# Kernel tuning notes

Hardware: AMD Instinct MI355X
Metric: run time of the kernel (lower is better)

## Reference

```python
import jax, jax.numpy as jnp
import numpy as np

M = 8      # num_modules
H = 128    # hidden_size per module
IN = 512   # input_size
MH = M * H

def _block_mask():
    # mask[mi*H:(mi+1)*H, mi*H:] = 1 (module mi reads modules >= mi)
    m = np.zeros((MH, MH), dtype=np.float32)
    for mi in range(M):
        m[mi*H:(mi+1)*H, mi*H:] = 1.0
    return jnp.asarray(m)

def _active_sizes(T):
    # number of active modules at step t: t=0 -> M, else min(M, trailing_zeros(t)+1)
    sizes = []
    for t in range(T):
        ma = 0
        while t % (2 ** ma) == 0 and ma < M:
            ma += 1
        sizes.append(ma * H)
    return jnp.asarray(np.array(sizes, dtype=np.int32))

def setup_inputs() -> dict:
    key = jax.random.key(0)
    k1, k2, k3, k4 = jax.random.split(key, 4)
    T, B = 256, 128
    scale = 1.0 / np.sqrt(MH)
    x = jax.random.normal(k1, (T, B, IN), dtype=jnp.float32)
    h_prev = jnp.zeros((B, MH), dtype=jnp.float32)
    Wxh = jax.random.normal(k2, (MH, IN), dtype=jnp.float32) * scale
    Whh = jax.random.normal(k3, (MH, MH), dtype=jnp.float32) * scale
    bh = jax.random.normal(k4, (MH,), dtype=jnp.float32) * scale
    return {"x": x, "h_prev": h_prev, "Wxh": Wxh, "Whh": Whh, "bh": bh}

def reference(x, h_prev, Wxh, Whh, bh):
    T = x.shape[0]
    mask = _block_mask()
    Whh_m = Whh * mask  # clockwork block-triangular mask, reapplied as in torch
    thresholds = _active_sizes(T)          # [T] active hidden width per step
    idx = jnp.arange(MH)

    # Precompute input projections for all timesteps: [T, B, MH]
    xW = jnp.einsum('tbi,hi->tbh', x, Wxh)

    def step(h, inp):
        xw_t, thr = inp
        # full-width update; rows < thr equal the torch sliced-matmul result
        h_full = h @ Whh_m.T + xw_t + bh
        h_new = jnp.where(idx < thr, h_full, h)
        return h_new, h_new

    h_last, out = jax.lax.scan(step, h_prev, (xW, thresholds))
    return (out, h_last)
```

## Files before the change

kernel.cpp:

```cpp
#include <hip/hip_runtime.h>
#include <hip/hip_bf16.h>


#define TT 256
#define BB 128
#define INW 512
#define HH 128
#define MHW 1024

typedef __bf16 bf16x8 __attribute__((ext_vector_type(8)));
typedef __bf16 bf16x4 __attribute__((ext_vector_type(4)));
typedef float f32x4 __attribute__((ext_vector_type(4)));

__constant__ unsigned int c_hmod_off[8] = {
    0u, 4194304u, 6291456u, 7340032u, 7864320u, 8126464u, 8257536u, 8323072u};

__device__ __forceinline__ int active_thr(int t) {
    int ma = (t == 0) ? 8 : min(__ffs(t), 8);
    return ma * HH;
}

__device__ __forceinline__ unsigned short f2bf(float f) {
    union { float f; unsigned int u; } v{f};
    unsigned int r = v.u + 0x7FFFu + ((v.u >> 16) & 1u);
    return (unsigned short)(r >> 16);
}
__device__ __forceinline__ unsigned int pack2(float lo, float hi) {
    return (unsigned int)f2bf(lo) | ((unsigned int)f2bf(hi) << 16);
}
__device__ __forceinline__ float bf2f(unsigned short u) {
    union { unsigned int i; float f; } v;
    v.i = ((unsigned int)u) << 16;
    return v.f;
}

__device__ __forceinline__ void gld_lds16(const void* g, char* l) {
    __builtin_amdgcn_global_load_lds(
        (const __attribute__((address_space(1))) void*)g,
        (__attribute__((address_space(3))) void*)l, 16, 0, 0);
}

__device__ __forceinline__ bf16x8 frag_ld(const char* tile, int row, int ks, int lane) {
    int off = (row * 128 + ks * 64 + (lane >> 4) * 16) ^ ((row & 7) << 4);
    return *reinterpret_cast<const bf16x8*>(tile + off);
}

__device__ __forceinline__ bf16x8 frag_ld_f32(const char* tile, int row, int ks, int g) {
    int off = ((row << 8) + ks * 128 + g * 32) ^ ((row & 7) << 4);
    f32x4 a = *reinterpret_cast<const f32x4*>(tile + off);
    f32x4 b = *reinterpret_cast<const f32x4*>(tile + (off ^ 16));
    bf16x8 u;
    u[0] = (__bf16)a[0]; u[1] = (__bf16)a[1]; u[2] = (__bf16)a[2]; u[3] = (__bf16)a[3];
    u[4] = (__bf16)b[0]; u[5] = (__bf16)b[1]; u[6] = (__bf16)b[2]; u[7] = (__bf16)b[3];
    return u;
}

__global__ __launch_bounds__(256) void k_xw(const float* __restrict__ x,
                                            const float* __restrict__ Wxh,
                                            const float* __restrict__ bh,
                                            float* __restrict__ xwb) {
    __shared__ char ldsW[2][32768];
    __shared__ char ldsX[2][16384];
    int id = blockIdx.x >> 1, half = blockIdx.x & 1;
    int rt = 0, rem = id;
    while (rem >= (256 >> rt)) { rem -= 256 >> rt; ++rt; }
    int t = rem << rt;

    int tid = threadIdx.x, lane = tid & 63, wid = tid >> 6;
    int l15 = lane & 15, g = lane >> 4;
    int wr = (wid >> 1) * 64, wc = (wid & 1) * 32;

    const float* gW[8];
    const float* gX[4];
    {
        int kb = (lane & 15) * 16;
#pragma unroll
        for (int i = 0; i < 8; ++i) {
            int row = i * 16 + wid * 4 + (lane >> 4);
            int kf = (kb ^ ((row & 7) << 4)) >> 2;
            gW[i] = Wxh + (size_t)(rt * 128 + row) * INW + kf;
        }
#pragma unroll
        for (int i = 0; i < 4; ++i) {
            int row = i * 16 + wid * 4 + (lane >> 4);
            int kf = (kb ^ ((row & 7) << 4)) >> 2;
            gX[i] = x + ((size_t)t * BB + half * 64 + row) * INW + kf;
        }
    }
#pragma unroll
    for (int i = 0; i < 8; ++i)
        gld_lds16(gW[i], &ldsW[0][0] + i * 4096 + wid * 1024);
#pragma unroll
    for (int i = 0; i < 4; ++i)
        gld_lds16(gX[i], &ldsX[0][0] + i * 4096 + wid * 1024);

    f32x4 acc[4][2] = {};
    for (int c = 0; c < 8; ++c) {
        int cur = c & 1;
        __syncthreads();
        if (c < 7) {
#pragma unroll
            for (int i = 0; i < 8; ++i)
                gld_lds16(gW[i] + (c + 1) * 64,
                          &ldsW[cur ^ 1][0] + i * 4096 + wid * 1024);
#pragma unroll
            for (int i = 0; i < 4; ++i)
                gld_lds16(gX[i] + (c + 1) * 64,
                          &ldsX[cur ^ 1][0] + i * 4096 + wid * 1024);
        }
#pragma unroll
        for (int ks = 0; ks < 2; ++ks) {
            bf16x8 fa[4], fb[2];
#pragma unroll
            for (int i = 0; i < 4; ++i)
                fa[i] = frag_ld_f32(&ldsW[cur][0], wr + i * 16 + l15, ks, g);
#pragma unroll
            for (int j = 0; j < 2; ++j)
                fb[j] = frag_ld_f32(&ldsX[cur][0], wc + j * 16 + l15, ks, g);
#pragma unroll
            for (int i = 0; i < 4; ++i)
#pragma unroll
                for (int j = 0; j < 2; ++j)
                    acc[i][j] = __builtin_amdgcn_mfma_f32_16x16x32_bf16(
                        fa[i], fb[j], acc[i][j], 0, 0, 0);
        }
    }
#pragma unroll
    for (int i = 0; i < 4; ++i) {
        int rbase = rt * 128 + wr + i * 16 + g * 4;
        float4 bias = *reinterpret_cast<const float4*>(&bh[rbase]);
#pragma unroll
        for (int j = 0; j < 2; ++j) {
            int b = half * 64 + wc + j * 16 + l15;
            float4 v = make_float4(acc[i][j][0] + bias.x, acc[i][j][1] + bias.y,
                                   acc[i][j][2] + bias.z, acc[i][j][3] + bias.w);
            *reinterpret_cast<float4*>(
                &xwb[(size_t)(t * BB + b) * MHW + rbase]) = v;
        }
    }
}

__global__ __launch_bounds__(256) void k_u(const float* __restrict__ Whh,
                                           const float* __restrict__ hprev,
                                           const unsigned short* __restrict__ hmod,
                                           float* __restrict__ xwb, int mi) {
    __shared__ char lds[131072];
    char* ldsA0 = lds;
    char* ldsA1 = lds + 32768;
    char* ldsH0 = lds + 65536;
    char* ldsH1 = lds + 98304;
    int k = blockIdx.x;
    int t = k << mi;
    int tid = threadIdx.x, lane = tid & 63, wid = tid >> 6;
    int l15 = lane & 15, g = lane >> 4;
    int wr = (wid >> 1) * 64, wc = (wid & 1) * 64;
    int ntile = 2 * (7 - mi);

    const float* gA[8];
    {
        int kb = l15 * 16;
#pragma unroll
        for (int i = 0; i < 8; ++i) {
            int row = i * 16 + wid * 4 + g;
            int kf = (kb ^ ((row & 7) << 4)) >> 2;
            gA[i] = Whh + (size_t)(mi * HH + row) * MHW + kf;
        }
    }
    f32x4 acc[4][4] = {};

    if (k == 0) {
        const float* gH[8];
        {
            int kb = l15 * 16;
#pragma unroll
            for (int i = 0; i < 8; ++i) {
                int row = i * 16 + wid * 4 + g;
                int kf = (kb ^ ((row & 7) << 4)) >> 2;
                gH[i] = hprev + (size_t)row * MHW + kf;
            }
        }
        auto stage = [&](int tt, char* dA, char* dH) {
            int j = mi + 1 + (tt >> 1), c0 = (tt & 1) * 64;
            int off = j * HH + c0;
#pragma unroll
            for (int i = 0; i < 8; ++i)
                gld_lds16(gA[i] + off, dA + i * 4096 + wid * 1024);
#pragma unroll
            for (int i = 0; i < 8; ++i)
                gld_lds16(gH[i] + off, dH + i * 4096 + wid * 1024);
        };
        stage(0, ldsA0, ldsH0);
        for (int tt = 0; tt < ntile; ++tt) {
            int cur = tt & 1;
            __syncthreads();
            if (tt + 1 < ntile)
                stage(tt + 1, cur ? ldsA0 : ldsA1, cur ? ldsH0 : ldsH1);
            const char* sA = cur ? ldsA1 : ldsA0;
            const char* sH = cur ? ldsH1 : ldsH0;
#pragma unroll
            for (int ks = 0; ks < 2; ++ks) {
                bf16x8 fa[4], fb[4];
#pragma unroll
                for (int i = 0; i < 4; ++i) {
                    fa[i] = frag_ld_f32(sA, wr + i * 16 + l15, ks, g);
                    fb[i] = frag_ld_f32(sH, wc + i * 16 + l15, ks, g);
                }
#pragma unroll
                for (int i = 0; i < 4; ++i)
#pragma unroll
                    for (int jj = 0; jj < 4; ++jj)
                        acc[i][jj] = __builtin_amdgcn_mfma_f32_16x16x32_bf16(
                            fa[i], fb[jj], acc[i][jj], 0, 0, 0);
            }
        }
    } else {
        size_t hoff[4];
        {
            int cb = ((lane & 7) * 16) ^ ((lane >> 3) << 4);
#pragma unroll
            for (int p = 0; p < 4; ++p) {
                int row = p * 32 + wid * 8 + (lane >> 3);
                hoff[p] = (size_t)row * HH + (cb >> 1);
            }
        }
        auto stage = [&](int tt, char* dA, char* dH) {
            int j = mi + 1 + (tt >> 1), c0 = (tt & 1) * 64;
            int offA = j * HH + c0;
#pragma unroll
            for (int i = 0; i < 8; ++i)
                gld_lds16(gA[i] + offA, dA + i * 4096 + wid * 1024);
            const unsigned short* hb =
                hmod + c_hmod_off[j] + (size_t)((t - 1) >> j) * BB * HH + c0;
#pragma unroll
            for (int p = 0; p < 4; ++p)
                gld_lds16(hb + hoff[p], dH + p * 4096 + wid * 1024);
        };
        stage(0, ldsA0, ldsH0);
        for (int tt = 0; tt < ntile; ++tt) {
            int cur = tt & 1;
            __syncthreads();
            if (tt + 1 < ntile)
                stage(tt + 1, cur ? ldsA0 : ldsA1, cur ? ldsH0 : ldsH1);
            const char* sA = cur ? ldsA1 : ldsA0;
            const char* sH = cur ? ldsH1 : ldsH0;
#pragma unroll
            for (int ks = 0; ks < 2; ++ks) {
                bf16x8 fa[4], fb[4];
#pragma unroll
                for (int i = 0; i < 4; ++i) {
                    fa[i] = frag_ld_f32(sA, wr + i * 16 + l15, ks, g);
                    fb[i] = frag_ld(sH, wc + i * 16 + l15, ks, lane);
                }
#pragma unroll
                for (int i = 0; i < 4; ++i)
#pragma unroll
                    for (int jj = 0; jj < 4; ++jj)
                        acc[i][jj] = __builtin_amdgcn_mfma_f32_16x16x32_bf16(
                            fa[i], fb[jj], acc[i][jj], 0, 0, 0);
            }
        }
    }
#pragma unroll
    for (int i = 0; i < 4; ++i) {
        int rbase = wr + i * 16 + g * 4;
#pragma unroll
        for (int j = 0; j < 4; ++j) {
            int b = wc + j * 16 + l15;
            float4* p = reinterpret_cast<float4*>(
                &xwb[(size_t)(t * BB + b) * MHW + mi * HH + rbase]);
            float4 v = *p;
            v.x += acc[i][j][0]; v.y += acc[i][j][1];
            v.z += acc[i][j][2]; v.w += acc[i][j][3];
            *p = v;
        }
    }
}

#define SYNC_LDS()                                              \
    do {                                                        \
        asm volatile("s_waitcnt lgkmcnt(0)" ::: "memory");      \
        __builtin_amdgcn_sched_barrier(0);                      \
        __builtin_amdgcn_s_barrier();                           \
        __builtin_amdgcn_sched_barrier(0);                      \
    } while (0)
#define SYNC_VM24()                                             \
    do {                                                        \
        asm volatile("s_waitcnt vmcnt(24)" ::: "memory");       \
        __builtin_amdgcn_sched_barrier(0);                      \
        __builtin_amdgcn_s_barrier();                           \
        __builtin_amdgcn_sched_barrier(0);                      \
    } while (0)

__global__ __launch_bounds__(256) void k_phase(const float* __restrict__ Whh,
                                               const float* __restrict__ hprev,
                                               const float* __restrict__ xwb,
                                               unsigned short* __restrict__ hmod,
                                               int mi) {
    int b0 = blockIdx.x * 16;
    int tid = threadIdx.x, lane = tid & 63, wid = tid >> 6;
    int l15 = lane & 15, g = lane >> 4;
    __shared__ char sH[2][4096];
    __shared__ char sU[8][8192];
    int Tm = TT >> mi;

    if (wid < 2) {
        bf16x8 Af[4][4];
        {
            const float* Ab = Whh + (size_t)(mi * HH) * MHW + mi * HH;
#pragma unroll
            for (int mm = 0; mm < 4; ++mm) {
                const float* row = Ab + (size_t)(64 * wid + mm * 16 + l15) * MHW;
#pragma unroll
                for (int kf = 0; kf < 4; ++kf) {
                    float4 v0 = *reinterpret_cast<const float4*>(row + kf * 32 + g * 8);
                    float4 v1 = *reinterpret_cast<const float4*>(row + kf * 32 + g * 8 + 4);
                    bf16x8 u;
                    u[0] = (__bf16)v0.x; u[1] = (__bf16)v0.y;
                    u[2] = (__bf16)v0.z; u[3] = (__bf16)v0.w;
                    u[4] = (__bf16)v1.x; u[5] = (__bf16)v1.y;
                    u[6] = (__bf16)v1.z; u[7] = (__bf16)v1.w;
                    Af[mm][kf] = u;
                }
            }
        }
#pragma unroll
        for (int p = 0; p < 2; ++p) {
            int tt = tid + p * 128;
            int b = tt >> 4, r8 = (tt & 15) * 8;
            const float* hp = hprev + (size_t)(b0 + b) * MHW + mi * HH + r8;
            float4 v0 = *reinterpret_cast<const float4*>(hp);
            float4 v1 = *reinterpret_cast<const float4*>(hp + 4);
            uint4 pk;
            pk.x = pack2(v0.x, v0.y); pk.y = pack2(v0.z, v0.w);
            pk.z = pack2(v1.x, v1.y); pk.w = pack2(v1.z, v1.w);
            int off = (b * 256 + r8 * 2) ^ ((b & 7) << 4);
            *reinterpret_cast<uint4*>(&sH[0][0] + off) = pk;
        }
        int roff[4], woff[4], uoff[4];
#pragma unroll
        for (int kf = 0; kf < 4; ++kf)
            roff[kf] = (l15 * 256 + kf * 64 + g * 16) ^ ((l15 & 7) << 4);
#pragma unroll
        for (int mm = 0; mm < 4; ++mm) {
            woff[mm] = (l15 * 256 + (64 * wid + mm * 16 + g * 4) * 2) ^ ((l15 & 7) << 4);
            uoff[mm] = (16 * wid + 4 * mm + g) * 256 + l15 * 16;
        }
        SYNC_LDS();

        for (int K = 0; K < Tm; ++K) {
            int cur = K & 1;
            const char* ub = &sU[K & 7][0];
            f32x4 acc[4], acc2[4];
#pragma unroll
            for (int mm = 0; mm < 4; ++mm) {
                acc[mm] = *reinterpret_cast<const f32x4*>(ub + uoff[mm]);
                acc2[mm] = (f32x4){0.f, 0.f, 0.f, 0.f};
            }
            bf16x8 Bf[4];
#pragma unroll
            for (int kf = 0; kf < 4; ++kf)
                Bf[kf] = *reinterpret_cast<const bf16x8*>(&sH[cur][0] + roff[kf]);
#pragma unroll
            for (int mm = 0; mm < 4; ++mm) {
                acc[mm] = __builtin_amdgcn_mfma_f32_16x16x32_bf16(
                    Af[mm][0], Bf[0], acc[mm], 0, 0, 0);
                acc2[mm] = __builtin_amdgcn_mfma_f32_16x16x32_bf16(
                    Af[mm][2], Bf[2], acc2[mm], 0, 0, 0);
                acc[mm] = __builtin_amdgcn_mfma_f32_16x16x32_bf16(
                    Af[mm][1], Bf[1], acc[mm], 0, 0, 0);
                acc2[mm] = __builtin_amdgcn_mfma_f32_16x16x32_bf16(
                    Af[mm][3], Bf[3], acc2[mm], 0, 0, 0);
            }
#pragma unroll
            for (int mm = 0; mm < 4; ++mm) {
                acc[mm] += acc2[mm];
                bf16x4 pk;
                pk[0] = (__bf16)acc[mm][0]; pk[1] = (__bf16)acc[mm][1];
                pk[2] = (__bf16)acc[mm][2]; pk[3] = (__bf16)acc[mm][3];
                *reinterpret_cast<bf16x4*>(&sH[cur ^ 1][0] + woff[mm]) = pk;
            }
            SYNC_LDS();
        }
    } else if (wid == 2) {
        const float* ubase = xwb + (size_t)(b0 + l15) * MHW + mi * HH + g * 4;
#pragma unroll
        for (int q = 0; q < 4; ++q) {
            int t = min(q, Tm - 1) << mi;
            const float* pt = ubase + (size_t)t * BB * MHW;
#pragma unroll
            for (int p = 0; p < 8; ++p)
                gld_lds16(pt + p * 16, &sU[q][0] + p * 1024);
        }
        SYNC_VM24();
        for (int K = 0; K < Tm; ++K) {
            int t = min(K + 4, Tm - 1) << mi;
            int slot = (K + 4) & 7;
            const float* pt = ubase + (size_t)t * BB * MHW;
#pragma unroll
            for (int p = 0; p < 8; ++p)
                gld_lds16(pt + p * 16, &sU[slot][0] + p * 1024);
            SYNC_VM24();
        }
        asm volatile("s_waitcnt vmcnt(0)" ::: "memory");
    } else {
        int bq = lane >> 2;
        int rr = (lane & 3) * 32;
        unsigned short* hm =
            hmod + c_hmod_off[mi] + (size_t)(b0 + bq) * HH + rr;
        int soff[4];
#pragma unroll
        for (int c = 0; c < 4; ++c)
            soff[c] = (bq * 256 + (rr + c * 8) * 2) ^ ((bq & 7) << 4);
        SYNC_LDS();
        for (int K = 0; K < Tm; ++K) {
            if (K >= 1) {
                uint4 h[4];
#pragma unroll
                for (int c = 0; c < 4; ++c)
                    h[c] = *reinterpret_cast<const uint4*>(&sH[K & 1][0] + soff[c]);
                unsigned short* dst = hm + (size_t)(K - 1) * BB * HH;
#pragma unroll
                for (int c = 0; c < 4; ++c)
                    *reinterpret_cast<uint4*>(dst + c * 8) = h[c];
            }
            SYNC_LDS();
        }
        {
            uint4 h[4];
#pragma unroll
            for (int c = 0; c < 4; ++c)
                h[c] = *reinterpret_cast<const uint4*>(&sH[Tm & 1][0] + soff[c]);
            unsigned short* dst = hm + (size_t)(Tm - 1) * BB * HH;
#pragma unroll
            for (int c = 0; c < 4; ++c)
                *reinterpret_cast<uint4*>(dst + c * 8) = h[c];
        }
    }
}

__global__ __launch_bounds__(256) void k_out(const unsigned short* __restrict__ hmod,
                                             float* __restrict__ out) {
    int b = blockIdx.x, t = blockIdx.y;
    int tid = threadIdx.x;
    int i = tid * 4;
    int j = i >> 7;
    int k = t >> j;
    ushort4 h = *reinterpret_cast<const ushort4*>(
        &hmod[c_hmod_off[j] + ((size_t)k * BB + b) * HH + (i & 127)]);
    float4 v = make_float4(bf2f(h.x), bf2f(h.y), bf2f(h.z), bf2f(h.w));
    *reinterpret_cast<float4*>(&out[((size_t)t * BB + b) * MHW + i]) = v;
    if (t == TT - 1) {
        *reinterpret_cast<float4*>(
            &out[(size_t)TT * BB * MHW + (size_t)b * MHW + i]) = v;
    }
}

extern "C" void kernel_launch(void* const* d_in, const int* in_sizes, int n_in,
                              void* d_out, int out_size, void* d_ws, size_t ws_size,
                              hipStream_t stream) {
    const float* x = (const float*)d_in[0];
    const float* hprev = (const float*)d_in[1];
    const float* Wxh = (const float*)d_in[2];
    const float* Whh = (const float*)d_in[3];
    const float* bh = (const float*)d_in[4];
    float* out = (float*)d_out;

    float* xwb = out;
    unsigned short* hmod = (unsigned short*)d_ws;

    k_xw<<<dim3(1020), 256, 0, stream>>>(x, Wxh, bh, xwb);

    for (int mi = 7; mi >= 0; --mi) {
        if (mi < 7)
            k_u<<<dim3(TT >> mi), 256, 0, stream>>>(Whh, hprev, hmod, xwb, mi);
        k_phase<<<8, 256, 0, stream>>>(Whh, hprev, xwb, hmod, mi);
    }

    k_out<<<dim3(128, 256), 256, 0, stream>>>(hmod, out);
}
```

Before: 404.1 us.

## Collapse recurrence into a single wave with a 16-slot hidden-state ring and page-level barriers

The sequential recurrence kernel now uses one compute wave instead of two. That wave holds all 8 row tiles of the diagonal Whh block in registers and issues its own xW prefetches. Hidden states go into a 16-slot LDS ring, so the writeback wave only has to synchronise once per page of up to 8 steps instead of every step. This removes a block-wide barrier from each step's critical path, at the cost of twice the register footprint per lane and half the MFMA parallelism per step.

```diff
diff --git a/kernel.cpp b/kernel.cpp
--- a/kernel.cpp
+++ b/kernel.cpp
@@ -11,6 +11,8 @@
 typedef __bf16 bf16x8 __attribute__((ext_vector_type(8)));
 typedef __bf16 bf16x4 __attribute__((ext_vector_type(4)));
 typedef float f32x4 __attribute__((ext_vector_type(4)));
+typedef unsigned int u32x2 __attribute__((ext_vector_type(2)));
+typedef __attribute__((address_space(3))) char lds_char;
 
 __constant__ unsigned int c_hmod_off[8] = {
     0u, 4194304u, 6291456u, 7340032u, 7864320u, 8126464u, 8257536u, 8323072u};
@@ -38,6 +40,20 @@
     __builtin_amdgcn_global_load_lds(
         (const __attribute__((address_space(1))) void*)g,
         (__attribute__((address_space(3))) void*)l, 16, 0, 0);
+}
+
+__device__ __forceinline__ f32x4 ds_read128_f(const lds_char* p) {
+    f32x4 r;
+    asm volatile("ds_read_b128 %0, %1" : "=v"(r) : "v"(p));
+    return r;
+}
+__device__ __forceinline__ bf16x8 ds_read128_h(const lds_char* p) {
+    bf16x8 r;
+    asm volatile("ds_read_b128 %0, %1" : "=v"(r) : "v"(p));
+    return r;
+}
+__device__ __forceinline__ void ds_write64(lds_char* p, u32x2 v) {
+    asm volatile("ds_write_b64 %0, %1" ::"v"(p), "v"(v) : "memory");
 }
 
 __device__ __forceinline__ bf16x8 frag_ld(const char* tile, int row, int ks, int lane) {
@@ -283,15 +299,8 @@
         __builtin_amdgcn_s_barrier();                           \
         __builtin_amdgcn_sched_barrier(0);                      \
     } while (0)
-#define SYNC_VM24()                                             \
-    do {                                                        \
-        asm volatile("s_waitcnt vmcnt(24)" ::: "memory");       \
-        __builtin_amdgcn_sched_barrier(0);                      \
-        __builtin_amdgcn_s_barrier();                           \
-        __builtin_amdgcn_sched_barrier(0);                      \
-    } while (0)
-
-__global__ __launch_bounds__(256) void k_phase(const float* __restrict__ Whh,
+
+__global__ __launch_bounds__(128) void k_phase(const float* __restrict__ Whh,
                                                const float* __restrict__ hprev,
                                                const float* __restrict__ xwb,
                                                unsigned short* __restrict__ hmod,
@@ -299,17 +308,18 @@
     int b0 = blockIdx.x * 16;
     int tid = threadIdx.x, lane = tid & 63, wid = tid >> 6;
     int l15 = lane & 15, g = lane >> 4;
-    __shared__ char sH[2][4096];
+    __shared__ char ring[16 * 4096];
     __shared__ char sU[8][8192];
     int Tm = TT >> mi;
-
-    if (wid < 2) {
-        bf16x8 Af[4][4];
+    int P = min(8, Tm);
+
+    if (wid == 0) {
+        bf16x8 Af[8][4];
         {
             const float* Ab = Whh + (size_t)(mi * HH) * MHW + mi * HH;
 #pragma unroll
-            for (int mm = 0; mm < 4; ++mm) {
-                const float* row = Ab + (size_t)(64 * wid + mm * 16 + l15) * MHW;
+            for (int m = 0; m < 8; ++m) {
+                const float* row = Ab + (size_t)(m * 16 + l15) * MHW;
 #pragma unroll
                 for (int kf = 0; kf < 4; ++kf) {
                     float4 v0 = *reinterpret_cast<const float4*>(row + kf * 32 + g * 8);
@@ -319,69 +329,33 @@
                     u[2] = (__bf16)v0.z; u[3] = (__bf16)v0.w;
                     u[4] = (__bf16)v1.x; u[5] = (__bf16)v1.y;
                     u[6] = (__bf16)v1.z; u[7] = (__bf16)v1.w;
-                    Af[mm][kf] = u;
+                    Af[m][kf] = u;
                 }
             }
         }
-#pragma unroll
-        for (int p = 0; p < 2; ++p) {
-            int tt = tid + p * 128;
-            int b = tt >> 4, r8 = (tt & 15) * 8;
-            const float* hp = hprev + (size_t)(b0 + b) * MHW + mi * HH + r8;
-            float4 v0 = *reinterpret_cast<const float4*>(hp);
-            float4 v1 = *reinterpret_cast<const float4*>(hp + 4);
-            uint4 pk;
-            pk.x = pack2(v0.x, v0.y); pk.y = pack2(v0.z, v0.w);
-            pk.z = pack2(v1.x, v1.y); pk.w = pack2(v1.z, v1.w);
-            int off = (b * 256 + r8 * 2) ^ ((b & 7) << 4);
-            *reinterpret_cast<uint4*>(&sH[0][0] + off) = pk;
-        }
-        int roff[4], woff[4], uoff[4];
+        int roff[4], woff[8], uoff[8];
 #pragma unroll
         for (int kf = 0; kf < 4; ++kf)
             roff[kf] = (l15 * 256 + kf * 64 + g * 16) ^ ((l15 & 7) << 4);
 #pragma unroll
-        for (int mm = 0; mm < 4; ++mm) {
-            woff[mm] = (l15 * 256 + (64 * wid + mm * 16 + g * 4) * 2) ^ ((l15 & 7) << 4);
-            uoff[mm] = (16 * wid + 4 * mm + g) * 256 + l15 * 16;
-        }
-        SYNC_LDS();
-
-        for (int K = 0; K < Tm; ++K) {
-            int cur = K & 1;
-            const char* ub = &sU[K & 7][0];
-            f32x4 acc[4], acc2[4];
-#pragma unroll
-            for (int mm = 0; mm < 4; ++mm) {
-                acc[mm] = *reinterpret_cast<const f32x4*>(ub + uoff[mm]);
-                acc2[mm] = (f32x4){0.f, 0.f, 0.f, 0.f};
-            }
-            bf16x8 Bf[4];
-#pragma unroll
-            for (int kf = 0; kf < 4; ++kf)
-                Bf[kf] = *reinterpret_cast<const bf16x8*>(&sH[cur][0] + roff[kf]);
-#pragma unroll
-            for (int mm = 0; mm < 4; ++mm) {
-                acc[mm] = __builtin_amdgcn_mfma_f32_16x16x32_bf16(
-                    Af[mm][0], Bf[0], acc[mm], 0, 0, 0);
-                acc2[mm] = __builtin_amdgcn_mfma_f32_16x16x32_bf16(
-                    Af[mm][2], Bf[2], acc2[mm], 0, 0, 0);
-                acc[mm] = __builtin_amdgcn_mfma_f32_16x16x32_bf16(
-                    Af[mm][1], Bf[1], acc[mm], 0, 0, 0);
-                acc2[mm] = __builtin_amdgcn_mfma_f32_16x16x32_bf16(
-                    Af[mm][3], Bf[3], acc2[mm], 0, 0, 0);
-            }
-#pragma unroll
-            for (int mm = 0; mm < 4; ++mm) {
-                acc[mm] += acc2[mm];
-                bf16x4 pk;
-                pk[0] = (__bf16)acc[mm][0]; pk[1] = (__bf16)acc[mm][1];
-                pk[2] = (__bf16)acc[mm][2]; pk[3] = (__bf16)acc[mm][3];
-                *reinterpret_cast<bf16x4*>(&sH[cur ^ 1][0] + woff[mm]) = pk;
-            }
-            SYNC_LDS();
-        }
-    } else if (wid == 2) {
+        for (int m = 0; m < 8; ++m) {
+            woff[m] = (l15 * 256 + (m * 16 + g * 4) * 2) ^ ((l15 & 7) << 4);
+            uoff[m] = (4 * m + g) * 256 + l15 * 16;
+        }
+        lds_char* ring3 = (lds_char*)&ring[0];
+        lds_char* su3 = (lds_char*)&sU[0][0];
+
+        {
+            const float* hp = hprev + (size_t)(b0 + l15) * MHW + mi * HH;
+#pragma unroll
+            for (int m = 0; m < 8; ++m) {
+                float4 v = *reinterpret_cast<const float4*>(hp + m * 16 + g * 4);
+                u32x2 pk;
+                pk[0] = pack2(v.x, v.y);
+                pk[1] = pack2(v.z, v.w);
+                ds_write64(ring3 + 15 * 4096 + woff[m], pk);
+            }
+        }
         const float* ubase = xwb + (size_t)(b0 + l15) * MHW + mi * HH + g * 4;
 #pragma unroll
         for (int q = 0; q < 4; ++q) {
@@ -391,49 +365,77 @@
             for (int p = 0; p < 8; ++p)
                 gld_lds16(pt + p * 16, &sU[q][0] + p * 1024);
         }
-        SYNC_VM24();
-        for (int K = 0; K < Tm; ++K) {
-            int t = min(K + 4, Tm - 1) << mi;
-            int slot = (K + 4) & 7;
-            const float* pt = ubase + (size_t)t * BB * MHW;
-#pragma unroll
-            for (int p = 0; p < 8; ++p)
-                gld_lds16(pt + p * 16, &sU[slot][0] + p * 1024);
-            SYNC_VM24();
-        }
-        asm volatile("s_waitcnt vmcnt(0)" ::: "memory");
+
+        for (int page = 0; page < Tm; page += P) {
+#pragma unroll 1
+            for (int s = 0; s < P; ++s) {
+                int K = page + s;
+                {
+                    int t = min(K + 4, Tm - 1) << mi;
+                    int slot = (K + 4) & 7;
+                    const float* pt = ubase + (size_t)t * BB * MHW;
+#pragma unroll
+                    for (int p = 0; p < 8; ++p)
+                        gld_lds16(pt + p * 16, &sU[slot][0] + p * 1024);
+                }
+                asm volatile("s_waitcnt vmcnt(32)" ::: "memory");
+                __builtin_amdgcn_sched_barrier(0);
+
+                const lds_char* ub = su3 + (K & 7) * 8192;
+                const lds_char* hin = ring3 + ((K + 15) & 15) * 4096;
+                lds_char* hout = ring3 + (K & 15) * 4096;
+
+                f32x4 acc[8];
+#pragma unroll
+                for (int m = 0; m < 8; ++m)
+                    acc[m] = ds_read128_f(ub + uoff[m]);
+                bf16x8 Bf[4];
+#pragma unroll
+                for (int kf = 0; kf < 4; ++kf)
+                    Bf[kf] = ds_read128_h(hin + roff[kf]);
+                asm volatile("s_waitcnt lgkmcnt(0)" ::: "memory");
+                __builtin_amdgcn_sched_barrier(0);
+
+#pragma unroll
+                for (int kf = 0; kf < 4; ++kf)
+#pragma unroll
+                    for (int m = 0; m < 8; ++m)
+                        acc[m] = __builtin_amdgcn_mfma_f32_16x16x32_bf16(
+                            Af[m][kf], Bf[kf], acc[m], 0, 0, 0);
+#pragma unroll
+                for (int m = 0; m < 8; ++m) {
+                    u32x2 pk;
+                    pk[0] = pack2(acc[m][0], acc[m][1]);
+                    pk[1] = pack2(acc[m][2], acc[m][3]);
+                    ds_write64(hout + woff[m], pk);
+                }
+            }
+            SYNC_LDS();
+        }
+        asm volatile("s_waitcnt vmcnt(0) lgkmcnt(0)" ::: "memory");
     } else {
         int bq = lane >> 2;
         int rr = (lane & 3) * 32;
-        unsigned short* hm =
-            hmod + c_hmod_off[mi] + (size_t)(b0 + bq) * HH + rr;
+        unsigned short* hm = hmod + c_hmod_off[mi] + (size_t)(b0 + bq) * HH + rr;
         int soff[4];
 #pragma unroll
         for (int c = 0; c < 4; ++c)
             soff[c] = (bq * 256 + (rr + c * 8) * 2) ^ ((bq & 7) << 4);
-        SYNC_LDS();
-        for (int K = 0; K < Tm; ++K) {
-            if (K >= 1) {
+        for (int page = 0; page < Tm; page += P) {
+            SYNC_LDS();
+#pragma unroll 1
+            for (int s = 0; s < P; ++s) {
+                int K = page + s;
+                const char* slot = &ring[(K & 15) * 4096];
                 uint4 h[4];
 #pragma unroll
                 for (int c = 0; c < 4; ++c)
-                    h[c] = *reinterpret_cast<const uint4*>(&sH[K & 1][0] + soff[c]);
-                unsigned short* dst = hm + (size_t)(K - 1) * BB * HH;
+                    h[c] = *reinterpret_cast<const uint4*>(slot + soff[c]);
+                unsigned short* dst = hm + (size_t)K * BB * HH;
 #pragma unroll
                 for (int c = 0; c < 4; ++c)
                     *reinterpret_cast<uint4*>(dst + c * 8) = h[c];
             }
-            SYNC_LDS();
-        }
-        {
-            uint4 h[4];
-#pragma unroll
-            for (int c = 0; c < 4; ++c)
-                h[c] = *reinterpret_cast<const uint4*>(&sH[Tm & 1][0] + soff[c]);
-            unsigned short* dst = hm + (size_t)(Tm - 1) * BB * HH;
-#pragma unroll
-            for (int c = 0; c < 4; ++c)
-                *reinterpret_cast<uint4*>(dst + c * 8) = h[c];
         }
     }
 }
@@ -473,7 +475,7 @@
     for (int mi = 7; mi >= 0; --mi) {
         if (mi < 7)
             k_u<<<dim3(TT >> mi), 256, 0, stream>>>(Whh, hprev, hmod, xwb, mi);
-        k_phase<<<8, 256, 0, stream>>>(Whh, hprev, xwb, hmod, mi);
+        k_phase<<<8, 128, 0, stream>>>(Whh, hprev, xwb, hmod, mi);
     }
 
     k_out<<<dim3(128, 256), 256, 0, stream>>>(hmod, out);
```

Result: slower. 583.9 us (+44.5%).

## Fuse per-module phase and update launches into one persistent dataflow megakernel

Applied to the files above, without the earlier changes.

Replaces the 15 alternating k_u/k_phase launches with a single persistent kernel. Eight blocks run the sequential recurrence for every module in turn. The remaining blocks pull update work items from an atomic counter and wait on page-level flags showing the hidden states they depend on are written. This lets the update matmuls of lower modules overlap with the recurrence of higher modules and removes launch gaps. The cost is spin-waiting, atomic flag traffic, and a deadlock risk if the 256 blocks are not all resident at once.

```diff
diff --git a/kernel.cpp b/kernel.cpp
--- a/kernel.cpp
+++ b/kernel.cpp
@@ -15,11 +15,6 @@
 __constant__ unsigned int c_hmod_off[8] = {
     0u, 4194304u, 6291456u, 7340032u, 7864320u, 8126464u, 8257536u, 8323072u};
 
-__device__ __forceinline__ int active_thr(int t) {
-    int ma = (t == 0) ? 8 : min(__ffs(t), 8);
-    return ma * HH;
-}
-
 __device__ __forceinline__ unsigned short f2bf(float f) {
     union { float f; unsigned int u; } v{f};
     unsigned int r = v.u + 0x7FFFu + ((v.u >> 16) & 1u);
@@ -38,6 +33,13 @@
     __builtin_amdgcn_global_load_lds(
         (const __attribute__((address_space(1))) void*)g,
         (__attribute__((address_space(3))) void*)l, 16, 0, 0);
+}
+
+__device__ __forceinline__ unsigned int aload(unsigned int* p) {
+    return __hip_atomic_load(p, __ATOMIC_RELAXED, __HIP_MEMORY_SCOPE_AGENT);
+}
+__device__ __forceinline__ void aadd(unsigned int* p, unsigned int v) {
+    __hip_atomic_fetch_add(p, v, __ATOMIC_RELAXED, __HIP_MEMORY_SCOPE_AGENT);
 }
 
 __device__ __forceinline__ bf16x8 frag_ld(const char* tile, int row, int ks, int lane) {
@@ -58,15 +60,20 @@
 __global__ __launch_bounds__(256) void k_xw(const float* __restrict__ x,
                                             const float* __restrict__ Wxh,
                                             const float* __restrict__ bh,
-                                            float* __restrict__ xwb) {
+                                            float* __restrict__ xwb,
+                                            unsigned int* __restrict__ flags) {
     __shared__ char ldsW[2][32768];
     __shared__ char ldsX[2][16384];
+    int tid = threadIdx.x;
+    if (blockIdx.x == 0) {
+        for (int i = tid; i < 2052; i += 256) flags[i] = 0u;
+    }
     int id = blockIdx.x >> 1, half = blockIdx.x & 1;
     int rt = 0, rem = id;
     while (rem >= (256 >> rt)) { rem -= 256 >> rt; ++rt; }
     int t = rem << rt;
 
-    int tid = threadIdx.x, lane = tid & 63, wid = tid >> 6;
+    int lane = tid & 63, wid = tid >> 6;
     int l15 = lane & 15, g = lane >> 4;
     int wr = (wid >> 1) * 64, wc = (wid & 1) * 32;
 
@@ -140,16 +147,14 @@
     }
 }
 
-__global__ __launch_bounds__(256) void k_u(const float* __restrict__ Whh,
-                                           const float* __restrict__ hprev,
-                                           const unsigned short* __restrict__ hmod,
-                                           float* __restrict__ xwb, int mi) {
-    __shared__ char lds[131072];
+__device__ void u_body(int mi, int k, const float* __restrict__ Whh,
+                       const float* __restrict__ hprev,
+                       const unsigned short* __restrict__ hmod,
+                       float* __restrict__ xwb, char* lds) {
     char* ldsA0 = lds;
     char* ldsA1 = lds + 32768;
     char* ldsH0 = lds + 65536;
     char* ldsH1 = lds + 98304;
-    int k = blockIdx.x;
     int t = k << mi;
     int tid = threadIdx.x, lane = tid & 63, wid = tid >> 6;
     int l15 = lane & 15, g = lane >> 4;
@@ -291,149 +296,224 @@
         __builtin_amdgcn_sched_barrier(0);                      \
     } while (0)
 
-__global__ __launch_bounds__(256) void k_phase(const float* __restrict__ Whh,
-                                               const float* __restrict__ hprev,
-                                               const float* __restrict__ xwb,
-                                               unsigned short* __restrict__ hmod,
-                                               int mi) {
-    int b0 = blockIdx.x * 16;
+__device__ __forceinline__ void item_of(int i, int& mi, int& k) {
+    if (i < 4) { mi = 6; k = i; }
+    else if (i < 12) { mi = 5; k = i - 4; }
+    else if (i < 28) { mi = 4; k = i - 12; }
+    else if (i < 60) { mi = 3; k = i - 28; }
+    else if (i < 124) { mi = 2; k = i - 60; }
+    else if (i < 252) { mi = 1; k = i - 124; }
+    else { mi = 0; k = i - 252; }
+}
+
+__global__ __launch_bounds__(256) void k_mega(const float* __restrict__ Whh,
+                                              const float* __restrict__ hprev,
+                                              float* __restrict__ xwb,
+                                              unsigned short* __restrict__ hmod,
+                                              unsigned int* __restrict__ flags) {
+    __shared__ char smem[131072];
+    __shared__ int s_item;
+    unsigned int* uflag = flags;
+    unsigned int* hpage = flags + 1792;
+    unsigned int* counter = flags + 2048;
     int tid = threadIdx.x, lane = tid & 63, wid = tid >> 6;
     int l15 = lane & 15, g = lane >> 4;
-    __shared__ char sH[2][4096];
-    __shared__ char sU[8][8192];
-    int Tm = TT >> mi;
-
-    if (wid < 2) {
-        bf16x8 Af[4][4];
-        {
-            const float* Ab = Whh + (size_t)(mi * HH) * MHW + mi * HH;
-#pragma unroll
-            for (int mm = 0; mm < 4; ++mm) {
-                const float* row = Ab + (size_t)(64 * wid + mm * 16 + l15) * MHW;
-#pragma unroll
-                for (int kf = 0; kf < 4; ++kf) {
-                    float4 v0 = *reinterpret_cast<const float4*>(row + kf * 32 + g * 8);
-                    float4 v1 = *reinterpret_cast<const float4*>(row + kf * 32 + g * 8 + 4);
-                    bf16x8 u;
-                    u[0] = (__bf16)v0.x; u[1] = (__bf16)v0.y;
-                    u[2] = (__bf16)v0.z; u[3] = (__bf16)v0.w;
-                    u[4] = (__bf16)v1.x; u[5] = (__bf16)v1.y;
-                    u[6] = (__bf16)v1.z; u[7] = (__bf16)v1.w;
-                    Af[mm][kf] = u;
-                }
-            }
-        }
-#pragma unroll
-        for (int p = 0; p < 2; ++p) {
-            int tt = tid + p * 128;
-            int b = tt >> 4, r8 = (tt & 15) * 8;
-            const float* hp = hprev + (size_t)(b0 + b) * MHW + mi * HH + r8;
-            float4 v0 = *reinterpret_cast<const float4*>(hp);
-            float4 v1 = *reinterpret_cast<const float4*>(hp + 4);
-            uint4 pk;
-            pk.x = pack2(v0.x, v0.y); pk.y = pack2(v0.z, v0.w);
-            pk.z = pack2(v1.x, v1.y); pk.w = pack2(v1.z, v1.w);
-            int off = (b * 256 + r8 * 2) ^ ((b & 7) << 4);
-            *reinterpret_cast<uint4*>(&sH[0][0] + off) = pk;
-        }
-        int roff[4], woff[4], uoff[4];
+
+    if (blockIdx.x < 8) {
+        int b0 = blockIdx.x * 16;
+        char* sH0 = smem;
+        char* sU0 = smem + 8192;
+
+        int roff[4], woff4[4], uoff4[4], soff[4];
 #pragma unroll
         for (int kf = 0; kf < 4; ++kf)
             roff[kf] = (l15 * 256 + kf * 64 + g * 16) ^ ((l15 & 7) << 4);
 #pragma unroll
         for (int mm = 0; mm < 4; ++mm) {
-            woff[mm] = (l15 * 256 + (64 * wid + mm * 16 + g * 4) * 2) ^ ((l15 & 7) << 4);
-            uoff[mm] = (16 * wid + 4 * mm + g) * 256 + l15 * 16;
-        }
-        SYNC_LDS();
-
-        for (int K = 0; K < Tm; ++K) {
-            int cur = K & 1;
-            const char* ub = &sU[K & 7][0];
-            f32x4 acc[4], acc2[4];
-#pragma unroll
-            for (int mm = 0; mm < 4; ++mm) {
-                acc[mm] = *reinterpret_cast<const f32x4*>(ub + uoff[mm]);
-                acc2[mm] = (f32x4){0.f, 0.f, 0.f, 0.f};
+            woff4[mm] = (l15 * 256 + (64 * (wid & 1) + mm * 16 + g * 4) * 2) ^ ((l15 & 7) << 4);
+            uoff4[mm] = (16 * (wid & 1) + 4 * mm + g) * 256 + l15 * 16;
+        }
+        {
+            int bq = lane >> 2, rr = (lane & 3) * 32;
+#pragma unroll
+            for (int c = 0; c < 4; ++c)
+                soff[c] = (bq * 256 + (rr + c * 8) * 2) ^ ((bq & 7) << 4);
+        }
+
+        for (int mi = 7; mi >= 0; --mi) {
+            int Tm = TT >> mi;
+            if (wid < 2) {
+                bf16x8 Af[4][4];
+                {
+                    const float* Ab = Whh + (size_t)(mi * HH) * MHW + mi * HH;
+#pragma unroll
+                    for (int mm = 0; mm < 4; ++mm) {
+                        const float* row = Ab + (size_t)(64 * wid + mm * 16 + l15) * MHW;
+#pragma unroll
+                        for (int kf = 0; kf < 4; ++kf) {
+                            float4 v0 = *reinterpret_cast<const float4*>(row + kf * 32 + g * 8);
+                            float4 v1 = *reinterpret_cast<const float4*>(row + kf * 32 + g * 8 + 4);
+                            bf16x8 u;
+                            u[0] = (__bf16)v0.x; u[1] = (__bf16)v0.y;
+                            u[2] = (__bf16)v0.z; u[3] = (__bf16)v0.w;
+                            u[4] = (__bf16)v1.x; u[5] = (__bf16)v1.y;
+                            u[6] = (__bf16)v1.z; u[7] = (__bf16)v1.w;
+                            Af[mm][kf] = u;
+                        }
+                    }
+                }
+#pragma unroll
+                for (int p = 0; p < 2; ++p) {
+                    int tt = tid + p * 128;
+                    int b = tt >> 4, r8 = (tt & 15) * 8;
+                    const float* hp = hprev + (size_t)(b0 + b) * MHW + mi * HH + r8;
+                    float4 v0 = *reinterpret_cast<const float4*>(hp);
+                    float4 v1 = *reinterpret_cast<const float4*>(hp + 4);
+                    uint4 pk;
+                    pk.x = pack2(v0.x, v0.y); pk.y = pack2(v0.z, v0.w);
+                    pk.z = pack2(v1.x, v1.y); pk.w = pack2(v1.z, v1.w);
+                    int off = (b * 256 + r8 * 2) ^ ((b & 7) << 4);
+                    *reinterpret_cast<uint4*>(sH0 + off) = pk;
+                }
+                SYNC_LDS();
+                for (int K = 0; K < Tm; ++K) {
+                    int cur = K & 1;
+                    const char* ub = sU0 + (K & 7) * 8192;
+                    f32x4 acc[4], acc2[4];
+#pragma unroll
+                    for (int mm = 0; mm < 4; ++mm) {
+                        acc[mm] = *reinterpret_cast<const f32x4*>(ub + uoff4[mm]);
+                        acc2[mm] = (f32x4){0.f, 0.f, 0.f, 0.f};
+                    }
+                    bf16x8 Bf[4];
+#pragma unroll
+                    for (int kf = 0; kf < 4; ++kf)
+                        Bf[kf] = *reinterpret_cast<const bf16x8*>(sH0 + cur * 4096 + roff[kf]);
+#pragma unroll
+                    for (int mm = 0; mm < 4; ++mm) {
+                        acc[mm] = __builtin_amdgcn_mfma_f32_16x16x32_bf16(
+                            Af[mm][0], Bf[0], acc[mm], 0, 0, 0);
+                        acc2[mm] = __builtin_amdgcn_mfma_f32_16x16x32_bf16(
+                            Af[mm][2], Bf[2], acc2[mm], 0, 0, 0);
+                        acc[mm] = __builtin_amdgcn_mfma_f32_16x16x32_bf16(
+                            Af[mm][1], Bf[1], acc[mm], 0, 0, 0);
+                        acc2[mm] = __builtin_amdgcn_mfma_f32_16x16x32_bf16(
+                            Af[mm][3], Bf[3], acc2[mm], 0, 0, 0);
+                    }
+#pragma unroll
+                    for (int mm = 0; mm < 4; ++mm) {
+                        acc[mm] += acc2[mm];
+                        bf16x4 pk;
+                        pk[0] = (__bf16)acc[mm][0]; pk[1] = (__bf16)acc[mm][1];
+                        pk[2] = (__bf16)acc[mm][2]; pk[3] = (__bf16)acc[mm][3];
+                        *reinterpret_cast<bf16x4*>(sH0 + (cur ^ 1) * 4096 + woff4[mm]) = pk;
+                    }
+                    SYNC_LDS();
+                }
+                SYNC_LDS();
+            } else if (wid == 2) {
+                const float* ubase = xwb + (size_t)(b0 + l15) * MHW + mi * HH + g * 4;
+                if (mi < 7) {
+                    int pmax = min(3, Tm - 1);
+                    for (int q = 0; q <= pmax; ++q)
+                        while (aload(&uflag[mi * 256 + q]) == 0u)
+                            __builtin_amdgcn_s_sleep(16);
+                }
+#pragma unroll
+                for (int q = 0; q < 4; ++q) {
+                    int t = min(q, Tm - 1) << mi;
+                    const float* pt = ubase + (size_t)t * BB * MHW;
+#pragma unroll
+                    for (int p = 0; p < 8; ++p)
+                        gld_lds16(pt + p * 16, sU0 + q * 8192 + p * 1024);
+                }
+                SYNC_VM24();
+                for (int K = 0; K < Tm; ++K) {
+                    int t = min(K + 4, Tm - 1) << mi;
+                    int slot = (K + 4) & 7;
+                    const float* pt = ubase + (size_t)t * BB * MHW;
+#pragma unroll
+                    for (int p = 0; p < 8; ++p)
+                        gld_lds16(pt + p * 16, sU0 + slot * 8192 + p * 1024);
+                    SYNC_VM24();
+                }
+                asm volatile("s_waitcnt vmcnt(0)" ::: "memory");
+                SYNC_LDS();
+            } else {
+                int bq = lane >> 2;
+                int rr = (lane & 3) * 32;
+                unsigned short* hm = hmod + c_hmod_off[mi] + (size_t)(b0 + bq) * HH + rr;
+                int verified = (mi < 7) ? -1 : (1 << 30);
+                auto verify = [&](int target) {
+                    while (verified < target) {
+                        if (aload(&uflag[mi * 256 + verified + 1]) != 0u) ++verified;
+                        else __builtin_amdgcn_s_sleep(16);
+                    }
+                };
+                if (mi < 7) verify(min(4, Tm - 1));
+                SYNC_LDS();
+                for (int K = 0; K < Tm; ++K) {
+                    if (mi < 7) verify(min(K + 5, Tm - 1));
+                    if (K >= 1) {
+                        int s = K - 1;
+                        uint4 h[4];
+#pragma unroll
+                        for (int c = 0; c < 4; ++c)
+                            h[c] = *reinterpret_cast<const uint4*>(
+                                smem + (K & 1) * 4096 + soff[c]);
+                        unsigned short* dst = hm + (size_t)s * BB * HH;
+#pragma unroll
+                        for (int c = 0; c < 4; ++c)
+                            *reinterpret_cast<uint4*>(dst + c * 8) = h[c];
+                        if (mi > 0 && (s & 7) == 7) {
+                            __threadfence();
+                            if (lane == 0) aadd(&hpage[mi * 32 + (s >> 3)], 1u);
+                        }
+                    }
+                    SYNC_LDS();
+                }
+                {
+                    uint4 h[4];
+#pragma unroll
+                    for (int c = 0; c < 4; ++c)
+                        h[c] = *reinterpret_cast<const uint4*>(
+                            smem + (Tm & 1) * 4096 + soff[c]);
+                    unsigned short* dst = hm + (size_t)(Tm - 1) * BB * HH;
+#pragma unroll
+                    for (int c = 0; c < 4; ++c)
+                        *reinterpret_cast<uint4*>(dst + c * 8) = h[c];
+                    if (mi > 0) {
+                        __threadfence();
+                        if (lane == 0) aadd(&hpage[mi * 32 + ((Tm - 1) >> 3)], 1u);
+                    }
+                }
+                SYNC_LDS();
             }
-            bf16x8 Bf[4];
-#pragma unroll
-            for (int kf = 0; kf < 4; ++kf)
-                Bf[kf] = *reinterpret_cast<const bf16x8*>(&sH[cur][0] + roff[kf]);
-#pragma unroll
-            for (int mm = 0; mm < 4; ++mm) {
-                acc[mm] = __builtin_amdgcn_mfma_f32_16x16x32_bf16(
-                    Af[mm][0], Bf[0], acc[mm], 0, 0, 0);
-                acc2[mm] = __builtin_amdgcn_mfma_f32_16x16x32_bf16(
-                    Af[mm][2], Bf[2], acc2[mm], 0, 0, 0);
-                acc[mm] = __builtin_amdgcn_mfma_f32_16x16x32_bf16(
-                    Af[mm][1], Bf[1], acc[mm], 0, 0, 0);
-                acc2[mm] = __builtin_amdgcn_mfma_f32_16x16x32_bf16(
-                    Af[mm][3], Bf[3], acc2[mm], 0, 0, 0);
+        }
+    } else {
+        for (;;) {
+            if (tid == 0)
+                s_item = (int)__hip_atomic_fetch_add(counter, 1u, __ATOMIC_RELAXED,
+                                                     __HIP_MEMORY_SCOPE_AGENT);
+            __syncthreads();
+            int i = s_item;
+            if (i >= 508) break;
+            int mi, k;
+            item_of(i, mi, k);
+            if (k > 0 && tid == 0) {
+                int t = k << mi;
+                for (int j = mi + 1; j < 8; ++j) {
+                    int pg = ((t - 1) >> j) >> 3;
+                    while (aload(&hpage[j * 32 + pg]) < 8u)
+                        __builtin_amdgcn_s_sleep(32);
+                }
             }
-#pragma unroll
-            for (int mm = 0; mm < 4; ++mm) {
-                acc[mm] += acc2[mm];
-                bf16x4 pk;
-                pk[0] = (__bf16)acc[mm][0]; pk[1] = (__bf16)acc[mm][1];
-                pk[2] = (__bf16)acc[mm][2]; pk[3] = (__bf16)acc[mm][3];
-                *reinterpret_cast<bf16x4*>(&sH[cur ^ 1][0] + woff[mm]) = pk;
-            }
-            SYNC_LDS();
-        }
-    } else if (wid == 2) {
-        const float* ubase = xwb + (size_t)(b0 + l15) * MHW + mi * HH + g * 4;
-#pragma unroll
-        for (int q = 0; q < 4; ++q) {
-            int t = min(q, Tm - 1) << mi;
-            const float* pt = ubase + (size_t)t * BB * MHW;
-#pragma unroll
-            for (int p = 0; p < 8; ++p)
-                gld_lds16(pt + p * 16, &sU[q][0] + p * 1024);
-        }
-        SYNC_VM24();
-        for (int K = 0; K < Tm; ++K) {
-            int t = min(K + 4, Tm - 1) << mi;
-            int slot = (K + 4) & 7;
-            const float* pt = ubase + (size_t)t * BB * MHW;
-#pragma unroll
-            for (int p = 0; p < 8; ++p)
-                gld_lds16(pt + p * 16, &sU[slot][0] + p * 1024);
-            SYNC_VM24();
-        }
-        asm volatile("s_waitcnt vmcnt(0)" ::: "memory");
-    } else {
-        int bq = lane >> 2;
-        int rr = (lane & 3) * 32;
-        unsigned short* hm =
-            hmod + c_hmod_off[mi] + (size_t)(b0 + bq) * HH + rr;
-        int soff[4];
-#pragma unroll
-        for (int c = 0; c < 4; ++c)
-            soff[c] = (bq * 256 + (rr + c * 8) * 2) ^ ((bq & 7) << 4);
-        SYNC_LDS();
-        for (int K = 0; K < Tm; ++K) {
-            if (K >= 1) {
-                uint4 h[4];
-#pragma unroll
-                for (int c = 0; c < 4; ++c)
-                    h[c] = *reinterpret_cast<const uint4*>(&sH[K & 1][0] + soff[c]);
-                unsigned short* dst = hm + (size_t)(K - 1) * BB * HH;
-#pragma unroll
-                for (int c = 0; c < 4; ++c)
-                    *reinterpret_cast<uint4*>(dst + c * 8) = h[c];
-            }
-            SYNC_LDS();
-        }
-        {
-            uint4 h[4];
-#pragma unroll
-            for (int c = 0; c < 4; ++c)
-                h[c] = *reinterpret_cast<const uint4*>(&sH[Tm & 1][0] + soff[c]);
-            unsigned short* dst = hm + (size_t)(Tm - 1) * BB * HH;
-#pragma unroll
-            for (int c = 0; c < 4; ++c)
-                *reinterpret_cast<uint4*>(dst + c * 8) = h[c];
+            __syncthreads();
+            u_body(mi, k, Whh, hprev, hmod, xwb, smem);
+            __threadfence();
+            __syncthreads();
+            if (tid == 0) aadd(&uflag[mi * 256 + k], 1u);
+            __syncthreads();
         }
     }
 }
@@ -467,14 +547,9 @@
 
     float* xwb = out;
     unsigned short* hmod = (unsigned short*)d_ws;
-
-    k_xw<<<dim3(1020), 256, 0, stream>>>(x, Wxh, bh, xwb);
-
-    for (int mi = 7; mi >= 0; --mi) {
-        if (mi < 7)
-            k_u<<<dim3(TT >> mi), 256, 0, stream>>>(Whh, hprev, hmod, xwb, mi);
-        k_phase<<<8, 256, 0, stream>>>(Whh, hprev, xwb, hmod, mi);
-    }
-
+    unsigned int* flags = (unsigned int*)((char*)d_ws + 16711680);
+
+    k_xw<<<dim3(1020), 256, 0, stream>>>(x, Wxh, bh, xwb, flags);
+    k_mega<<<dim3(256), 256, 0, stream>>>(Whh, hprev, xwb, hmod, flags);
     k_out<<<dim3(128, 256), 256, 0, stream>>>(hmod, out);
 }
```

New measurement: 506.7 us. 1.25x slower.
